# Kernel tuning notes

Measured on AMD Instinct MI355X. Metric: run time of the kernel, lower is better.

Reference implementation:

```python
import jax, jax.numpy as jnp
from jax import lax
import numpy as np
import math

B, T, IN_DIM, HID = 2048, 20, 600, 1024


def setup_inputs() -> dict:
    key = jax.random.key(0)
    kx, k1, k2, k3, k4 = jax.random.split(key, 5)
    std = 1.0 / math.sqrt(HID)  # reset_parameters: uniform(-std, std)
    x = jax.random.normal(kx, (B, T, IN_DIM), dtype=jnp.float32)
    W_ih = jax.random.uniform(k1, (3 * HID, IN_DIM), minval=-std, maxval=std, dtype=jnp.float32)
    b_ih = jax.random.uniform(k2, (3 * HID,), minval=-std, maxval=std, dtype=jnp.float32)
    W_hh = jax.random.uniform(k3, (3 * HID, HID), minval=-std, maxval=std, dtype=jnp.float32)
    b_hh = jax.random.uniform(k4, (3 * HID,), minval=-std, maxval=std, dtype=jnp.float32)
    return {"x": x, "W_ih": W_ih, "b_ih": b_ih, "W_hh": W_hh, "b_hh": b_hh}


def reference(x, W_ih, b_ih, W_hh, b_hh):
    # x: [B, T, in_dim]; returns last hidden state [B, HID]
    batch = x.shape[0]
    hid = W_hh.shape[1]
    # Precompute input-side gate projections for all timesteps (same math as per-step Linear)
    gate_x = jnp.einsum('btd,gd->btg', x, W_ih) + b_ih  # [B, T, 3H]

    def step(h, gxt):
        gate_h = h @ W_hh.T + b_hh  # [B, 3H]
        i_r, i_i, i_n = jnp.split(gxt, 3, axis=1)
        h_r, h_i, h_n = jnp.split(gate_h, 3, axis=1)
        resetgate = jax.nn.sigmoid(i_r + h_r)
        inputgate = jax.nn.sigmoid(i_i + h_i)
        newgate = jnp.tanh(i_n + resetgate * h_n)
        hy = newgate + inputgate * (h - newgate)
        return hy, None

    h0 = jnp.zeros((batch, hid), dtype=x.dtype)
    hT, _ = lax.scan(step, h0, jnp.swapaxes(gate_x, 0, 1))  # scan over time [T, B, 3H]
    return hT
```

## Files before the change

### kernel.cpp

```cpp
#include <hip/hip_runtime.h>
#include <hip/hip_bf16.h>
#include <math.h>

#define HID   1024
#define IN_D  600
#define IN_DP 608
#define BATCH 2048
#define TSTEP 20
#define BT    (BATCH * TSTEP)
#define G3    3072

typedef __attribute__((ext_vector_type(8))) short bf16x8;
typedef __attribute__((ext_vector_type(4))) float f32x4;

#define GLB(p) ((const __attribute__((address_space(1))) void*)(p))
#define LDS(p) ((__attribute__((address_space(3))) void*)(p))

__device__ __forceinline__ short f2bf(float f) {
    __hip_bfloat16 b = __float2bfloat16(f);
    return *(short*)&b;
}
__device__ __forceinline__ float bf2f(short s) {
    __hip_bfloat16 b = *(__hip_bfloat16*)&s;
    return __bfloat162float(b);
}

__global__ __launch_bounds__(256) void gemm_input(const short* __restrict__ X,
                                                  const short* __restrict__ W,
                                                  const float* __restrict__ b_ih,
                                                  short* __restrict__ gx) {
    __shared__ short sA[128 * 32];
    __shared__ short sB[128 * 32];

    const int id    = blockIdx.x;
    const int xcd   = id & 7;
    const int local = id >> 3;
    const int nsub  = local % 3;
    const int mblk  = local / 3;
    const int m0 = mblk * 128;
    const int n0 = (xcd * 3 + nsub) * 128;

    const int tid  = threadIdx.x;
    const int wave = tid >> 6;
    const int lane = tid & 63;
    const int wm = (wave >> 1) * 64;
    const int wn = (wave & 1) * 64;

    const int srow = tid >> 2;
    const int scol = (tid & 3) * 8;
    const int fm = lane & 15;
    const int fq = lane >> 4;

    f32x4 acc[4][4] = {};

    for (int k0 = 0; k0 < IN_DP; k0 += 32) {
#pragma unroll
        for (int j = 0; j < 2; ++j) {
            const short* ga = X + (size_t)(m0 + j * 64 + srow) * IN_DP + k0 + scol;
            __builtin_amdgcn_global_load_lds(GLB(ga), LDS(sA + j * 2048 + wave * 512), 16, 0, 0);
            const short* gb = W + (size_t)(n0 + j * 64 + srow) * IN_DP + k0 + scol;
            __builtin_amdgcn_global_load_lds(GLB(gb), LDS(sB + j * 2048 + wave * 512), 16, 0, 0);
        }
        __syncthreads();

        bf16x8 af[4], bf[4];
#pragma unroll
        for (int mi = 0; mi < 4; ++mi)
            af[mi] = *(const bf16x8*)(sA + (wm + mi * 16 + fm) * 32 + fq * 8);
#pragma unroll
        for (int ni = 0; ni < 4; ++ni)
            bf[ni] = *(const bf16x8*)(sB + (wn + ni * 16 + fm) * 32 + fq * 8);
#pragma unroll
        for (int mi = 0; mi < 4; ++mi)
#pragma unroll
            for (int ni = 0; ni < 4; ++ni)
                acc[mi][ni] = __builtin_amdgcn_mfma_f32_16x16x32_bf16(af[mi], bf[ni], acc[mi][ni], 0, 0, 0);
        __syncthreads();
    }

#pragma unroll
    for (int ni = 0; ni < 4; ++ni) {
        int gn = n0 + wn + ni * 16 + fm;
        float bias = b_ih[gn];
#pragma unroll
        for (int mi = 0; mi < 4; ++mi) {
#pragma unroll
            for (int r = 0; r < 4; ++r) {
                int gm = m0 + wm + mi * 16 + fq * 4 + r;
                gx[(size_t)gm * G3 + gn] = f2bf(acc[mi][ni][r] + bias);
            }
        }
    }
}

__global__ __launch_bounds__(512) void gru_step(const short* __restrict__ hb_in,
                                                const short* __restrict__ Wr,
                                                const short* __restrict__ gx,
                                                const float* __restrict__ b_hh,
                                                short* __restrict__ hb_out,
                                                float* __restrict__ out,
                                                int t, int last) {
    __shared__ short LDSF[4 * 20480];

    const int id   = blockIdx.x;
    const int xcd  = id & 7;
    const int rest = id >> 3;
    const int jsub = rest & 1;
    const int mblk = rest >> 1;
    const int j0 = (xcd * 2 + jsub) * 64;
    const int m0 = mblk * 128;
    const int hchunk = j0 >> 6;

    const int tid  = threadIdx.x;
    const int wave = tid >> 6;
    const int lane = tid & 63;
    const int wm = (wave >> 2) * 64;
    const int jg = wave & 3;
    const int fm = lane & 15;
    const int fq = lane >> 4;

    const int srow8 = lane >> 3;
    const int sxor  = ((lane & 7) ^ srow8) * 8;

    const short* Wblk = Wr + (size_t)(j0 * 3) * HID;
    const short* gxt  = gx + (size_t)t * BATCH * G3;

    f32x4 acc[4][3] = {};
    short hsnap[4][4];

    auto stage = [&](int kc, int bsel) {
        int k0 = kc * 64;
        short* base = LDSF + bsel * 20480;
#pragma unroll
        for (int i = 0; i < 2; ++i) {
            int row0 = wave * 16 + i * 8;
            const short* g = hb_in + (size_t)(m0 + row0 + srow8) * HID + k0 + sxor;
            __builtin_amdgcn_global_load_lds(GLB(g), LDS(base + row0 * 64), 16, 0, 0);
        }
#pragma unroll
        for (int i = 0; i < 3; ++i) {
            int row0 = wave * 24 + i * 8;
            const short* g = Wblk + (size_t)(row0 + srow8) * HID + k0 + sxor;
            __builtin_amdgcn_global_load_lds(GLB(g), LDS(base + 8192 + row0 * 64), 16, 0, 0);
        }
    };
    auto sgx_load = [&](int q) {
        int g = q >> 4;
        int row0 = (q & 15) * 8;
        const short* src = gxt + (size_t)(m0 + row0 + srow8) * G3 + g * HID + j0 + sxor;
        __builtin_amdgcn_global_load_lds(GLB(src), LDS(LDSF + q * 512), 16, 0, 0);
    };

    const int jj = jg * 16 + fm;

    stage(0, 0);
    stage(1, 1);

#pragma unroll
    for (int ic = 0; ic < 16; ++ic) {
        if (ic < 14) {
            stage(ic + 2, (ic + 2) & 3);
        } else if (ic == 14) {
#pragma unroll
            for (int i = 0; i < 5; ++i) sgx_load(wave * 5 + i);
        } else {
            sgx_load(40 + wave);
        }
        if (ic < 15) asm volatile("s_waitcnt vmcnt(10)" : : : "memory");
        else         asm volatile("s_waitcnt vmcnt(6)"  : : : "memory");
        __builtin_amdgcn_s_barrier();
        __builtin_amdgcn_sched_barrier(0);

        short* buf = LDSF + (ic & 3) * 20480;

        if (ic == hchunk) {
#pragma unroll
            for (int mi = 0; mi < 4; ++mi)
#pragma unroll
                for (int r = 0; r < 4; ++r) {
                    int mrow = wm + mi * 16 + fq * 4 + r;
                    hsnap[mi][r] = buf[mrow * 64 + (jj ^ ((mrow & 7) * 8))];
                }
        }

#pragma unroll
        for (int kk = 0; kk < 2; ++kk) {
            bf16x8 af[4], bg[3];
            const int cbase = kk * 32 + fq * 8;
            const int csw = cbase ^ ((fm & 7) * 8);
#pragma unroll
            for (int mi = 0; mi < 4; ++mi)
                af[mi] = *(const bf16x8*)(&buf[(wm + mi * 16 + fm) * 64 + csw]);
#pragma unroll
            for (int g = 0; g < 3; ++g)
                bg[g] = *(const bf16x8*)(&buf[8192 + (jg * 48 + g * 16 + fm) * 64 + csw]);
            __builtin_amdgcn_s_setprio(1);
#pragma unroll
            for (int mi = 0; mi < 4; ++mi)
#pragma unroll
                for (int g = 0; g < 3; ++g)
                    acc[mi][g] = __builtin_amdgcn_mfma_f32_16x16x32_bf16(af[mi], bg[g], acc[mi][g], 0, 0, 0);
            __builtin_amdgcn_s_setprio(0);
        }
    }

    asm volatile("s_waitcnt vmcnt(0)" : : : "memory");
    __builtin_amdgcn_s_barrier();
    __builtin_amdgcn_sched_barrier(0);

    const short* sGX = LDSF;
    const int jlane = j0 + jj;
    const float bh_r = b_hh[jlane];
    const float bh_i = b_hh[HID + jlane];
    const float bh_n = b_hh[2 * HID + jlane];

#pragma unroll
    for (int mi = 0; mi < 4; ++mi) {
#pragma unroll
        for (int r = 0; r < 4; ++r) {
            int mloc = wm + mi * 16 + fq * 4 + r;
            int gm = m0 + mloc;
            int jsw = jj ^ ((mloc & 7) * 8);
            float xr = bf2f(sGX[        mloc * 64 + jsw]);
            float xi = bf2f(sGX[ 8192 + mloc * 64 + jsw]);
            float xn = bf2f(sGX[16384 + mloc * 64 + jsw]);

            float rg = 1.0f / (1.0f + __expf(-(xr + acc[mi][0][r] + bh_r)));
            float ig = 1.0f / (1.0f + __expf(-(xi + acc[mi][1][r] + bh_i)));
            float ng = tanhf(xn + rg * (acc[mi][2][r] + bh_n));

            float h  = bf2f(hsnap[mi][r]);
            float hy = ng + ig * (h - ng);
            size_t idx = (size_t)gm * HID + jlane;
            hb_out[idx] = f2bf(hy);
            if (last) out[idx] = hy;
        }
    }
}

__global__ __launch_bounds__(256) void cvt_x(const float* __restrict__ X, short* __restrict__ Xb) {
    int rd = blockIdx.x;
    int tt = rd >> 11;
    int b  = rd & (BATCH - 1);
    const float* s = X + ((size_t)b * TSTEP + tt) * IN_D;
    short* d = Xb + (size_t)rd * IN_DP;
    for (int c = threadIdx.x; c < IN_DP; c += 256)
        d[c] = (c < IN_D) ? f2bf(s[c]) : (short)0;
}

__global__ __launch_bounds__(256) void cvt_wih(const float* __restrict__ W, short* __restrict__ Wb) {
    int r = blockIdx.x;
    for (int c = threadIdx.x; c < IN_DP; c += 256) {
        float v = (c < IN_D) ? W[(size_t)r * IN_D + c] : 0.f;
        Wb[(size_t)r * IN_DP + c] = f2bf(v);
    }
}

__global__ __launch_bounds__(256) void cvt_whh(const float* __restrict__ W, short* __restrict__ Wr) {
    int n  = blockIdx.x;
    int jb = n / 48;
    int rem = n - jb * 48;
    int g  = rem >> 4;
    int ji = rem & 15;
    const float* s = W + (size_t)(g * HID + jb * 16 + ji) * HID;
    short* d = Wr + (size_t)n * HID;
    for (int c = threadIdx.x; c < HID; c += 256) d[c] = f2bf(s[c]);
}

extern "C" void kernel_launch(void* const* d_in, const int* in_sizes, int n_in,
                              void* d_out, int out_size, void* d_ws, size_t ws_size,
                              hipStream_t stream) {
    const float* x    = (const float*)d_in[0];
    const float* W_ih = (const float*)d_in[1];
    const float* b_ih = (const float*)d_in[2];
    const float* W_hh = (const float*)d_in[3];
    const float* b_hh = (const float*)d_in[4];
    float* out = (float*)d_out;

    char* p = (char*)d_ws;
    short* gx     = (short*)p;  p += (size_t)BT * G3 * 2;
    short* x_bf   = (short*)p;  p += (size_t)BT * IN_DP * 2;
    short* hb0    = (short*)p;  p += (size_t)BATCH * HID * 2;
    short* hb1    = (short*)p;  p += (size_t)BATCH * HID * 2;
    short* Wih_bf = (short*)p;  p += (size_t)G3 * IN_DP * 2;
    short* Whh_r  = (short*)p;  p += (size_t)G3 * HID * 2;

    cvt_wih<<<G3, 256, 0, stream>>>(W_ih, Wih_bf);
    cvt_whh<<<G3, 256, 0, stream>>>(W_hh, Whh_r);
    cvt_x<<<BT, 256, 0, stream>>>(x, x_bf);
    hipMemsetAsync(hb0, 0, (size_t)BATCH * HID * 2, stream);

    gemm_input<<<7680, 256, 0, stream>>>(x_bf, Wih_bf, b_ih, gx);

    for (int t = 0; t < TSTEP; ++t) {
        const short* hin = (t & 1) ? hb1 : hb0;
        short* hout      = (t & 1) ? hb0 : hb1;
        gru_step<<<256, 512, 0, stream>>>(hin, Whh_r, gx, b_hh,
                                          hout, out, t, t == TSTEP - 1 ? 1 : 0);
    }
}
```

Before: 839.1 us.

## Fuse all GRU timesteps into one persistent kernel with grid barrier

Replaces the 20 per-timestep gru_step launches with one persistent kernel of 256 blocks that loops over time. Blocks synchronise between steps through an atomic counter per timestep in workspace memory. Each block prefetches its first two W_hh tiles before waiting on the barrier, so those weight loads overlap the wait. This removes the cost of launching a kernel per step, but it requires all 256 blocks to be resident at once and adds the spin-wait barrier.

```diff
diff --git a/kernel.cpp b/kernel.cpp
--- a/kernel.cpp
+++ b/kernel.cpp
@@ -93,13 +93,12 @@
     }
 }
 
-__global__ __launch_bounds__(512) void gru_step(const short* __restrict__ hb_in,
-                                                const short* __restrict__ Wr,
-                                                const short* __restrict__ gx,
-                                                const float* __restrict__ b_hh,
-                                                short* __restrict__ hb_out,
-                                                float* __restrict__ out,
-                                                int t, int last) {
+__global__ __launch_bounds__(512) void gru_fused(short* hb0, short* hb1,
+                                                 const short* __restrict__ Wr,
+                                                 const short* __restrict__ gx,
+                                                 const float* __restrict__ b_hh,
+                                                 float* __restrict__ out,
+                                                 unsigned* __restrict__ cnt) {
     __shared__ short LDSF[4 * 20480];
 
     const int id   = blockIdx.x;
@@ -123,117 +122,145 @@
     const int sxor  = ((lane & 7) ^ srow8) * 8;
 
     const short* Wblk = Wr + (size_t)(j0 * 3) * HID;
-    const short* gxt  = gx + (size_t)t * BATCH * G3;
-
-    f32x4 acc[4][3] = {};
-    short hsnap[4][4];
-
-    auto stage = [&](int kc, int bsel) {
-        int k0 = kc * 64;
-        short* base = LDSF + bsel * 20480;
-#pragma unroll
-        for (int i = 0; i < 2; ++i) {
-            int row0 = wave * 16 + i * 8;
-            const short* g = hb_in + (size_t)(m0 + row0 + srow8) * HID + k0 + sxor;
-            __builtin_amdgcn_global_load_lds(GLB(g), LDS(base + row0 * 64), 16, 0, 0);
-        }
-#pragma unroll
-        for (int i = 0; i < 3; ++i) {
-            int row0 = wave * 24 + i * 8;
-            const short* g = Wblk + (size_t)(row0 + srow8) * HID + k0 + sxor;
-            __builtin_amdgcn_global_load_lds(GLB(g), LDS(base + 8192 + row0 * 64), 16, 0, 0);
-        }
-    };
-    auto sgx_load = [&](int q) {
-        int g = q >> 4;
-        int row0 = (q & 15) * 8;
-        const short* src = gxt + (size_t)(m0 + row0 + srow8) * G3 + g * HID + j0 + sxor;
-        __builtin_amdgcn_global_load_lds(GLB(src), LDS(LDSF + q * 512), 16, 0, 0);
-    };
-
     const int jj = jg * 16 + fm;
-
-    stage(0, 0);
-    stage(1, 1);
-
-#pragma unroll
-    for (int ic = 0; ic < 16; ++ic) {
-        if (ic < 14) {
-            stage(ic + 2, (ic + 2) & 3);
-        } else if (ic == 14) {
-#pragma unroll
-            for (int i = 0; i < 5; ++i) sgx_load(wave * 5 + i);
-        } else {
-            sgx_load(40 + wave);
-        }
-        if (ic < 15) asm volatile("s_waitcnt vmcnt(10)" : : : "memory");
-        else         asm volatile("s_waitcnt vmcnt(6)"  : : : "memory");
-        __builtin_amdgcn_s_barrier();
-        __builtin_amdgcn_sched_barrier(0);
-
-        short* buf = LDSF + (ic & 3) * 20480;
-
-        if (ic == hchunk) {
-#pragma unroll
-            for (int mi = 0; mi < 4; ++mi)
-#pragma unroll
-                for (int r = 0; r < 4; ++r) {
-                    int mrow = wm + mi * 16 + fq * 4 + r;
-                    hsnap[mi][r] = buf[mrow * 64 + (jj ^ ((mrow & 7) * 8))];
-                }
-        }
-
-#pragma unroll
-        for (int kk = 0; kk < 2; ++kk) {
-            bf16x8 af[4], bg[3];
-            const int cbase = kk * 32 + fq * 8;
-            const int csw = cbase ^ ((fm & 7) * 8);
-#pragma unroll
-            for (int mi = 0; mi < 4; ++mi)
-                af[mi] = *(const bf16x8*)(&buf[(wm + mi * 16 + fm) * 64 + csw]);
-#pragma unroll
-            for (int g = 0; g < 3; ++g)
-                bg[g] = *(const bf16x8*)(&buf[8192 + (jg * 48 + g * 16 + fm) * 64 + csw]);
-            __builtin_amdgcn_s_setprio(1);
-#pragma unroll
-            for (int mi = 0; mi < 4; ++mi)
-#pragma unroll
-                for (int g = 0; g < 3; ++g)
-                    acc[mi][g] = __builtin_amdgcn_mfma_f32_16x16x32_bf16(af[mi], bg[g], acc[mi][g], 0, 0, 0);
-            __builtin_amdgcn_s_setprio(0);
-        }
-    }
-
-    asm volatile("s_waitcnt vmcnt(0)" : : : "memory");
-    __builtin_amdgcn_s_barrier();
-    __builtin_amdgcn_sched_barrier(0);
-
-    const short* sGX = LDSF;
     const int jlane = j0 + jj;
     const float bh_r = b_hh[jlane];
     const float bh_i = b_hh[HID + jlane];
     const float bh_n = b_hh[2 * HID + jlane];
 
-#pragma unroll
-    for (int mi = 0; mi < 4; ++mi) {
-#pragma unroll
-        for (int r = 0; r < 4; ++r) {
-            int mloc = wm + mi * 16 + fq * 4 + r;
-            int gm = m0 + mloc;
-            int jsw = jj ^ ((mloc & 7) * 8);
-            float xr = bf2f(sGX[        mloc * 64 + jsw]);
-            float xi = bf2f(sGX[ 8192 + mloc * 64 + jsw]);
-            float xn = bf2f(sGX[16384 + mloc * 64 + jsw]);
-
-            float rg = 1.0f / (1.0f + __expf(-(xr + acc[mi][0][r] + bh_r)));
-            float ig = 1.0f / (1.0f + __expf(-(xi + acc[mi][1][r] + bh_i)));
-            float ng = tanhf(xn + rg * (acc[mi][2][r] + bh_n));
-
-            float h  = bf2f(hsnap[mi][r]);
-            float hy = ng + ig * (h - ng);
-            size_t idx = (size_t)gm * HID + jlane;
-            hb_out[idx] = f2bf(hy);
-            if (last) out[idx] = hy;
+#pragma unroll 1
+    for (int t = 0; t < TSTEP; ++t) {
+        const short* hin  = (t & 1) ? hb1 : hb0;
+        short*       hout = (t & 1) ? hb0 : hb1;
+        const short* gxt  = gx + (size_t)t * BATCH * G3;
+
+        auto stageW = [&](int kc, int bsel) {
+            int k0 = kc * 64;
+            short* base = LDSF + bsel * 20480;
+#pragma unroll
+            for (int i = 0; i < 3; ++i) {
+                int row0 = wave * 24 + i * 8;
+                const short* g = Wblk + (size_t)(row0 + srow8) * HID + k0 + sxor;
+                __builtin_amdgcn_global_load_lds(GLB(g), LDS(base + 8192 + row0 * 64), 16, 0, 0);
+            }
+        };
+        auto stageH = [&](int kc, int bsel) {
+            int k0 = kc * 64;
+            short* base = LDSF + bsel * 20480;
+#pragma unroll
+            for (int i = 0; i < 2; ++i) {
+                int row0 = wave * 16 + i * 8;
+                const short* g = hin + (size_t)(m0 + row0 + srow8) * HID + k0 + sxor;
+                __builtin_amdgcn_global_load_lds(GLB(g), LDS(base + row0 * 64), 16, 0, 0);
+            }
+        };
+        auto stage = [&](int kc, int bsel) { stageH(kc, bsel); stageW(kc, bsel); };
+        auto sgx_load = [&](int q) {
+            int g = q >> 4;
+            int row0 = (q & 15) * 8;
+            const short* src = gxt + (size_t)(m0 + row0 + srow8) * G3 + g * HID + j0 + sxor;
+            __builtin_amdgcn_global_load_lds(GLB(src), LDS(LDSF + q * 512), 16, 0, 0);
+        };
+
+        stageW(0, 0);
+        stageW(1, 1);
+        if (t > 0) {
+            if (tid == 0) {
+                __hip_atomic_fetch_add(&cnt[t], 1u, __ATOMIC_RELAXED,
+                                       __HIP_MEMORY_SCOPE_AGENT);
+                while (__hip_atomic_load(&cnt[t], __ATOMIC_RELAXED,
+                                         __HIP_MEMORY_SCOPE_AGENT) < 256u)
+                    __builtin_amdgcn_s_sleep(2);
+            }
+            __syncthreads();
+            __threadfence();
+        }
+        stageH(0, 0);
+        stageH(1, 1);
+
+        f32x4 acc[4][3] = {};
+        short hsnap[4][4];
+
+#pragma unroll
+        for (int ic = 0; ic < 16; ++ic) {
+            if (ic < 14) {
+                stage(ic + 2, (ic + 2) & 3);
+            } else if (ic == 14) {
+#pragma unroll
+                for (int i = 0; i < 5; ++i) sgx_load(wave * 5 + i);
+            } else {
+                sgx_load(40 + wave);
+            }
+            if (ic == 0)       asm volatile("s_waitcnt vmcnt(7)"  : : : "memory");
+            else if (ic < 15)  asm volatile("s_waitcnt vmcnt(10)" : : : "memory");
+            else               asm volatile("s_waitcnt vmcnt(6)"  : : : "memory");
+            __builtin_amdgcn_s_barrier();
+            __builtin_amdgcn_sched_barrier(0);
+
+            short* buf = LDSF + (ic & 3) * 20480;
+
+            if (ic == hchunk) {
+#pragma unroll
+                for (int mi = 0; mi < 4; ++mi)
+#pragma unroll
+                    for (int r = 0; r < 4; ++r) {
+                        int mrow = wm + mi * 16 + fq * 4 + r;
+                        hsnap[mi][r] = buf[mrow * 64 + (jj ^ ((mrow & 7) * 8))];
+                    }
+            }
+
+#pragma unroll
+            for (int kk = 0; kk < 2; ++kk) {
+                bf16x8 af[4], bg[3];
+                const int cbase = kk * 32 + fq * 8;
+                const int csw = cbase ^ ((fm & 7) * 8);
+#pragma unroll
+                for (int mi = 0; mi < 4; ++mi)
+                    af[mi] = *(const bf16x8*)(&buf[(wm + mi * 16 + fm) * 64 + csw]);
+#pragma unroll
+                for (int g = 0; g < 3; ++g)
+                    bg[g] = *(const bf16x8*)(&buf[8192 + (jg * 48 + g * 16 + fm) * 64 + csw]);
+                __builtin_amdgcn_s_setprio(1);
+#pragma unroll
+                for (int mi = 0; mi < 4; ++mi)
+#pragma unroll
+                    for (int g = 0; g < 3; ++g)
+                        acc[mi][g] = __builtin_amdgcn_mfma_f32_16x16x32_bf16(af[mi], bg[g], acc[mi][g], 0, 0, 0);
+                __builtin_amdgcn_s_setprio(0);
+            }
+        }
+
+        asm volatile("s_waitcnt vmcnt(0)" : : : "memory");
+        __builtin_amdgcn_s_barrier();
+        __builtin_amdgcn_sched_barrier(0);
+
+        const short* sGX = LDSF;
+#pragma unroll
+        for (int mi = 0; mi < 4; ++mi) {
+#pragma unroll
+            for (int r = 0; r < 4; ++r) {
+                int mloc = wm + mi * 16 + fq * 4 + r;
+                int gm = m0 + mloc;
+                int jsw = jj ^ ((mloc & 7) * 8);
+                float xr = bf2f(sGX[        mloc * 64 + jsw]);
+                float xi = bf2f(sGX[ 8192 + mloc * 64 + jsw]);
+                float xn = bf2f(sGX[16384 + mloc * 64 + jsw]);
+
+                float rg = 1.0f / (1.0f + __expf(-(xr + acc[mi][0][r] + bh_r)));
+                float ig = 1.0f / (1.0f + __expf(-(xi + acc[mi][1][r] + bh_i)));
+                float ng = tanhf(xn + rg * (acc[mi][2][r] + bh_n));
+
+                float h  = bf2f(hsnap[mi][r]);
+                float hy = ng + ig * (h - ng);
+                size_t idx = (size_t)gm * HID + jlane;
+                hout[idx] = f2bf(hy);
+                if (t == TSTEP - 1) out[idx] = hy;
+            }
+        }
+
+        if (t < TSTEP - 1) {
+            __threadfence();
+            __syncthreads();
         }
     }
 }
@@ -284,18 +311,15 @@
     short* hb1    = (short*)p;  p += (size_t)BATCH * HID * 2;
     short* Wih_bf = (short*)p;  p += (size_t)G3 * IN_DP * 2;
     short* Whh_r  = (short*)p;  p += (size_t)G3 * HID * 2;
+    unsigned* bar = (unsigned*)p; p += 256;
 
     cvt_wih<<<G3, 256, 0, stream>>>(W_ih, Wih_bf);
     cvt_whh<<<G3, 256, 0, stream>>>(W_hh, Whh_r);
     cvt_x<<<BT, 256, 0, stream>>>(x, x_bf);
     hipMemsetAsync(hb0, 0, (size_t)BATCH * HID * 2, stream);
+    hipMemsetAsync(bar, 0, 256, stream);
 
     gemm_input<<<7680, 256, 0, stream>>>(x_bf, Wih_bf, b_ih, gx);
 
-    for (int t = 0; t < TSTEP; ++t) {
-        const short* hin = (t & 1) ? hb1 : hb0;
-        short* hout      = (t & 1) ? hb0 : hb1;
-        gru_step<<<256, 512, 0, stream>>>(hin, Whh_r, gx, b_hh,
-                                          hout, out, t, t == TSTEP - 1 ? 1 : 0);
-    }
-}
+    gru_fused<<<256, 512, 0, stream>>>(hb0, hb1, Whh_r, gx, b_hh, out, bar);
+}
```

Result: slower. 2.604 ms (+210.3%).

## Rewrite input-projection GEMM with 4-stage LDS pipeline and gate-interleaved weights

Applied to the files above, without the earlier changes.

Replaces the input-side GEMM with a 512-thread kernel that streams 64-wide K chunks through a 4-deep LDS ring buffer, using XOR-swizzled layout and explicit vmcnt waits so loads overlap MFMA work. W_ih is reordered so each block computes all three gates for a 64-column slice, matching the recurrent weight layout. K padding grows to 640 to fit the 64-wide chunks, which adds some wasted compute and traffic. The recurrent steps dominate total time, so the GEMM is only a fraction of the kernel time.

```diff
diff --git a/kernel.cpp b/kernel.cpp
--- a/kernel.cpp
+++ b/kernel.cpp
@@ -4,7 +4,7 @@
 
 #define HID   1024
 #define IN_D  600
-#define IN_DP 608
+#define IN_DP 640
 #define BATCH 2048
 #define TSTEP 20
 #define BT    (BATCH * TSTEP)
@@ -25,69 +25,97 @@
     return __bfloat162float(b);
 }
 
-__global__ __launch_bounds__(256) void gemm_input(const short* __restrict__ X,
-                                                  const short* __restrict__ W,
-                                                  const float* __restrict__ b_ih,
-                                                  short* __restrict__ gx) {
-    __shared__ short sA[128 * 32];
-    __shared__ short sB[128 * 32];
+__global__ __launch_bounds__(512) void gemm_input2(const short* __restrict__ X,
+                                                   const short* __restrict__ Wih_r,
+                                                   const float* __restrict__ b_ih,
+                                                   short* __restrict__ gx) {
+    __shared__ short LDSF[4 * 20480];
 
     const int id    = blockIdx.x;
     const int xcd   = id & 7;
     const int local = id >> 3;
-    const int nsub  = local % 3;
-    const int mblk  = local / 3;
+    const int jsub  = local & 1;
+    const int mblk  = local >> 1;
+    const int j0 = (xcd * 2 + jsub) * 64;
     const int m0 = mblk * 128;
-    const int n0 = (xcd * 3 + nsub) * 128;
 
     const int tid  = threadIdx.x;
     const int wave = tid >> 6;
     const int lane = tid & 63;
-    const int wm = (wave >> 1) * 64;
-    const int wn = (wave & 1) * 64;
-
-    const int srow = tid >> 2;
-    const int scol = (tid & 3) * 8;
+    const int wm = (wave >> 2) * 64;
+    const int jg = wave & 3;
     const int fm = lane & 15;
     const int fq = lane >> 4;
 
-    f32x4 acc[4][4] = {};
-
-    for (int k0 = 0; k0 < IN_DP; k0 += 32) {
-#pragma unroll
-        for (int j = 0; j < 2; ++j) {
-            const short* ga = X + (size_t)(m0 + j * 64 + srow) * IN_DP + k0 + scol;
-            __builtin_amdgcn_global_load_lds(GLB(ga), LDS(sA + j * 2048 + wave * 512), 16, 0, 0);
-            const short* gb = W + (size_t)(n0 + j * 64 + srow) * IN_DP + k0 + scol;
-            __builtin_amdgcn_global_load_lds(GLB(gb), LDS(sB + j * 2048 + wave * 512), 16, 0, 0);
-        }
-        __syncthreads();
-
-        bf16x8 af[4], bf[4];
-#pragma unroll
-        for (int mi = 0; mi < 4; ++mi)
-            af[mi] = *(const bf16x8*)(sA + (wm + mi * 16 + fm) * 32 + fq * 8);
-#pragma unroll
-        for (int ni = 0; ni < 4; ++ni)
-            bf[ni] = *(const bf16x8*)(sB + (wn + ni * 16 + fm) * 32 + fq * 8);
-#pragma unroll
-        for (int mi = 0; mi < 4; ++mi)
-#pragma unroll
-            for (int ni = 0; ni < 4; ++ni)
-                acc[mi][ni] = __builtin_amdgcn_mfma_f32_16x16x32_bf16(af[mi], bf[ni], acc[mi][ni], 0, 0, 0);
-        __syncthreads();
-    }
-
-#pragma unroll
-    for (int ni = 0; ni < 4; ++ni) {
-        int gn = n0 + wn + ni * 16 + fm;
-        float bias = b_ih[gn];
+    const int srow8 = lane >> 3;
+    const int sxor  = ((lane & 7) ^ srow8) * 8;
+
+    const short* Wblk = Wih_r + (size_t)(j0 * 3) * IN_DP;
+
+    f32x4 acc[4][3] = {};
+
+    auto stage = [&](int kc, int bsel) {
+        int k0 = kc * 64;
+        short* base = LDSF + bsel * 20480;
+#pragma unroll
+        for (int i = 0; i < 2; ++i) {
+            int row0 = wave * 16 + i * 8;
+            const short* g = X + (size_t)(m0 + row0 + srow8) * IN_DP + k0 + sxor;
+            __builtin_amdgcn_global_load_lds(GLB(g), LDS(base + row0 * 64), 16, 0, 0);
+        }
+#pragma unroll
+        for (int i = 0; i < 3; ++i) {
+            int row0 = wave * 24 + i * 8;
+            const short* g = Wblk + (size_t)(row0 + srow8) * IN_DP + k0 + sxor;
+            __builtin_amdgcn_global_load_lds(GLB(g), LDS(base + 8192 + row0 * 64), 16, 0, 0);
+        }
+    };
+
+    stage(0, 0);
+    stage(1, 1);
+
+#pragma unroll
+    for (int ic = 0; ic < 10; ++ic) {
+        if (ic < 8) stage(ic + 2, (ic + 2) & 3);
+        if (ic < 8)       asm volatile("s_waitcnt vmcnt(10)" : : : "memory");
+        else if (ic == 8) asm volatile("s_waitcnt vmcnt(5)"  : : : "memory");
+        else              asm volatile("s_waitcnt vmcnt(0)"  : : : "memory");
+        __builtin_amdgcn_s_barrier();
+        __builtin_amdgcn_sched_barrier(0);
+
+        short* buf = LDSF + (ic & 3) * 20480;
+
+#pragma unroll
+        for (int kk = 0; kk < 2; ++kk) {
+            bf16x8 af[4], bg[3];
+            const int cbase = kk * 32 + fq * 8;
+            const int csw = cbase ^ ((fm & 7) * 8);
+#pragma unroll
+            for (int mi = 0; mi < 4; ++mi)
+                af[mi] = *(const bf16x8*)(&buf[(wm + mi * 16 + fm) * 64 + csw]);
+#pragma unroll
+            for (int g = 0; g < 3; ++g)
+                bg[g] = *(const bf16x8*)(&buf[8192 + (jg * 48 + g * 16 + fm) * 64 + csw]);
+            __builtin_amdgcn_s_setprio(1);
+#pragma unroll
+            for (int mi = 0; mi < 4; ++mi)
+#pragma unroll
+                for (int g = 0; g < 3; ++g)
+                    acc[mi][g] = __builtin_amdgcn_mfma_f32_16x16x32_bf16(af[mi], bg[g], acc[mi][g], 0, 0, 0);
+            __builtin_amdgcn_s_setprio(0);
+        }
+    }
+
+    const int jl = j0 + jg * 16 + fm;
+#pragma unroll
+    for (int g = 0; g < 3; ++g) {
+        float bias = b_ih[g * HID + jl];
 #pragma unroll
         for (int mi = 0; mi < 4; ++mi) {
 #pragma unroll
             for (int r = 0; r < 4; ++r) {
                 int gm = m0 + wm + mi * 16 + fq * 4 + r;
-                gx[(size_t)gm * G3 + gn] = f2bf(acc[mi][ni][r] + bias);
+                gx[(size_t)gm * G3 + g * HID + jl] = f2bf(acc[mi][g][r] + bias);
             }
         }
     }
@@ -248,12 +276,16 @@
         d[c] = (c < IN_D) ? f2bf(s[c]) : (short)0;
 }
 
-__global__ __launch_bounds__(256) void cvt_wih(const float* __restrict__ W, short* __restrict__ Wb) {
-    int r = blockIdx.x;
-    for (int c = threadIdx.x; c < IN_DP; c += 256) {
-        float v = (c < IN_D) ? W[(size_t)r * IN_D + c] : 0.f;
-        Wb[(size_t)r * IN_DP + c] = f2bf(v);
-    }
+__global__ __launch_bounds__(256) void cvt_wih_r(const float* __restrict__ W, short* __restrict__ Wb) {
+    int n  = blockIdx.x;
+    int jb = n / 48;
+    int rem = n - jb * 48;
+    int g  = rem >> 4;
+    int ji = rem & 15;
+    const float* s = W + (size_t)(g * HID + jb * 16 + ji) * IN_D;
+    short* d = Wb + (size_t)n * IN_DP;
+    for (int c = threadIdx.x; c < IN_DP; c += 256)
+        d[c] = (c < IN_D) ? f2bf(s[c]) : (short)0;
 }
 
 __global__ __launch_bounds__(256) void cvt_whh(const float* __restrict__ W, short* __restrict__ Wr) {
@@ -282,15 +314,15 @@
     short* x_bf   = (short*)p;  p += (size_t)BT * IN_DP * 2;
     short* hb0    = (short*)p;  p += (size_t)BATCH * HID * 2;
     short* hb1    = (short*)p;  p += (size_t)BATCH * HID * 2;
-    short* Wih_bf = (short*)p;  p += (size_t)G3 * IN_DP * 2;
+    short* Wih_r  = (short*)p;  p += (size_t)G3 * IN_DP * 2;
     short* Whh_r  = (short*)p;  p += (size_t)G3 * HID * 2;
 
-    cvt_wih<<<G3, 256, 0, stream>>>(W_ih, Wih_bf);
+    cvt_wih_r<<<G3, 256, 0, stream>>>(W_ih, Wih_r);
     cvt_whh<<<G3, 256, 0, stream>>>(W_hh, Whh_r);
     cvt_x<<<BT, 256, 0, stream>>>(x, x_bf);
     hipMemsetAsync(hb0, 0, (size_t)BATCH * HID * 2, stream);
 
-    gemm_input<<<7680, 256, 0, stream>>>(x_bf, Wih_bf, b_ih, gx);
+    gemm_input2<<<5120, 512, 0, stream>>>(x_bf, Wih_r, b_ih, gx);
 
     for (int t = 0; t < TSTEP; ++t) {
         const short* hin = (t & 1) ? hb1 : hb0;
```

Result: faster. 795.1 us (-5.2%).
